# Kernel tuning notes

Measured on AMD Instinct MI355X. Metric: run time of the kernel, lower is better.

## Reference

```python
import jax, jax.numpy as jnp
import numpy as np

H, W = 512, 512
CHUNK = 128            # gaussians blended per scan step
BLUR = 0.3             # antialiasing dilation (as in 3DGS EWA low-pass)
ALPHA_MIN = 1.0 / 255.0
ALPHA_MAX = 0.99


def setup_inputs() -> dict:
    key = jax.random.key(0)
    k = jax.random.split(key, 6)
    N = 8192
    means2D = jax.random.uniform(k[0], (N, 2), jnp.float32) * jnp.array([W, H], jnp.float32)
    colors = jax.random.uniform(k[1], (N, 3), jnp.float32)
    opacities = jax.random.uniform(k[2], (N, 1), jnp.float32)
    scales = jax.random.uniform(k[3], (N, 2), jnp.float32) * 15.0 + 1.0   # pixels
    rotations = jax.random.uniform(k[4], (N, 1), jnp.float32) * (2.0 * np.pi)
    depths = jax.random.uniform(k[5], (N,), jnp.float32)
    background = jnp.zeros((3,), jnp.float32)
    return dict(means2D=means2D, colors=colors, opacities=opacities,
                scales=scales, rotations=rotations, depths=depths,
                background=background)


def _rasterize(means2D, colors, opacities, scales, rotations, depths, background):
    # depth sort: front (small depth) first
    order = jnp.argsort(depths)
    m = means2D[order]                 # [N,2] (x,y)
    col = colors[order]                # [N,3]
    op = opacities[order][:, 0]        # [N]
    s = scales[order]                  # [N,2]
    th = rotations[order][:, 0]        # [N]

    # 2D covariance  Sigma = R diag(s^2) R^T
    c, si = jnp.cos(th), jnp.sin(th)
    sx2, sy2 = s[:, 0] ** 2, s[:, 1] ** 2
    A = c * c * sx2 + si * si * sy2
    Cc = si * si * sx2 + c * c * sy2
    B = c * si * (sx2 - sy2)
    det = A * Cc - B * B
    # antialiasing: dilate covariance, compensate opacity
    A2, C2 = A + BLUR, Cc + BLUR
    det2 = A2 * C2 - B * B
    op = op * jnp.sqrt(jnp.maximum(det / det2, 0.0))
    invdet = 1.0 / det2
    ia, ib, ic = C2 * invdet, -B * invdet, A2 * invdet   # Sigma^-1 entries

    # pixel centers
    ys, xs = jnp.meshgrid(jnp.arange(H, dtype=jnp.float32) + 0.5,
                          jnp.arange(W, dtype=jnp.float32) + 0.5, indexing='ij')

    N = m.shape[0]
    nchunk = N // CHUNK
    chunk = lambda a: a.reshape((nchunk, CHUNK) + a.shape[1:])
    gs = (chunk(m), chunk(col), chunk(op), chunk(ia), chunk(ib), chunk(ic))

    def step(carry, g):
        T, acc = carry                       # T:[H,W] transmittance, acc:[3,H,W]
        gm, gcol, gop, gia, gib, gic = g     # per-chunk [C,...]
        dx = xs[None] - gm[:, 0, None, None]                 # [C,H,W]
        dy = ys[None] - gm[:, 1, None, None]
        power = (-0.5 * (gia[:, None, None] * dx * dx + gic[:, None, None] * dy * dy)
                 - gib[:, None, None] * dx * dy)
        alpha = jnp.minimum(ALPHA_MAX, gop[:, None, None] * jnp.exp(power))
        alpha = jnp.where(alpha < ALPHA_MIN, 0.0, alpha)     # skip tiny splats (as CUDA)
        one_m = 1.0 - alpha
        cum = jnp.cumprod(one_m, axis=0)                     # inclusive
        Twithin = jnp.concatenate([jnp.ones_like(cum[:1]), cum[:-1]], 0)  # exclusive
        w = alpha * Twithin * T[None]                        # blend weight per gaussian
        acc = acc + jnp.einsum('nc,nhw->chw', gcol, w)
        T = T * cum[-1]
        return (T, acc), None

    init = (jnp.ones((H, W), jnp.float32), jnp.zeros((3, H, W), jnp.float32))
    (T, acc), _ = jax.lax.scan(step, init, gs)
    color = acc + background[:, None, None] * T[None]        # [3,H,W]
    return color


def reference(means2D, colors, opacities, scales, rotations, depths, background):
    return _rasterize(means2D, colors, opacities, scales, rotations, depths, background)
```

## Files before the change

kernel.cpp:

```cpp
#include <hip/hip_runtime.h>
#include <hip/hip_fp16.h>
#include <stdint.h>

#define HH 512
#define WW 512
#define NPIX (HH*WW)
#define ALPHA_MIN_C (1.0f/255.0f)
#define ALPHA_MAX_C 0.99f
#define BLUR_C 0.3f
#define TERM_EPS 1.0e-4f
#define LOG2E 1.4426950408889634f

#define JSL 512
__global__ __launch_bounds__(256) void rank_kernel(const float* __restrict__ depths,
                                                   int N, int* __restrict__ partial) {
    __shared__ uint32_t sk[JSL];
    const int tid = threadIdx.x;
    const int ngb = N >> 8;
    const int gb = blockIdx.x % ngb;
    const int jb = blockIdx.x / ngb;
    const int j0 = jb * JSL;
    for (int i = tid; i < JSL; i += 256)
        sk[i] = __float_as_uint(depths[j0 + i]);
    __syncthreads();
    const int g = gb * 256 + tid;
    const uint32_t mb = __float_as_uint(depths[g]);
    const int glim = g - j0;
    int cnt = 0;
    const uint4* sk4 = (const uint4*)sk;
#pragma unroll 8
    for (int q = 0; q < JSL / 4; ++q) {
        uint4 v = sk4[q];
        const int i4 = q * 4;
        cnt += (v.x < mb) || (v.x == mb && (i4 + 0) < glim);
        cnt += (v.y < mb) || (v.y == mb && (i4 + 1) < glim);
        cnt += (v.z < mb) || (v.z == mb && (i4 + 2) < glim);
        cnt += (v.w < mb) || (v.w == mb && (i4 + 3) < glim);
    }
    partial[jb * N + g] = cnt;
}

__global__ __launch_bounds__(256) void prep_kernel(
    const float* __restrict__ means, const float* __restrict__ colors,
    const float* __restrict__ ops, const float* __restrict__ scales,
    const float* __restrict__ rots, const int* __restrict__ partial, int N,
    float4* __restrict__ pP, float4* __restrict__ pQ, float* __restrict__ pC) {
    int g = blockIdx.x * 256 + threadIdx.x;
    if (g >= N) return;
    int pos = 0;
#pragma unroll
    for (int s = 0; s < 16; ++s) pos += partial[s * N + g];
    float mx = means[2*g], my = means[2*g+1];
    float th = rots[g];
    float c = cosf(th), si = sinf(th);
    float sx = scales[2*g], sy = scales[2*g+1];
    float sx2 = sx*sx, sy2 = sy*sy;
    float A  = c*c*sx2 + si*si*sy2;
    float Cc = si*si*sx2 + c*c*sy2;
    float B  = c*si*(sx2 - sy2);
    float det = A*Cc - B*B;
    float A2 = A + BLUR_C, C2 = Cc + BLUR_C;
    float det2 = A2*C2 - B*B;
    float op = ops[g] * sqrtf(fmaxf(det/det2, 0.0f));
    float invd = 1.0f/det2;
    float ia = C2*invd, ib = -B*invd, ic = A2*invd;
    float iaF = -0.5f*LOG2E*ia, icF = -0.5f*LOG2E*ic, ibF = -LOG2E*ib;
    float bx, by, lop;
    if (op < ALPHA_MIN_C) {
        bx = -1.0f; by = -1.0f; lop = -128.0f;
    } else {
        float t = __logf(op * 255.0f);
        bx = sqrtf(fmaxf(2.0f * t * A2, 0.0f)) * 1.0001f + 0.1f;
        by = sqrtf(fmaxf(2.0f * t * C2, 0.0f)) * 1.0001f + 0.1f;
        lop = __log2f(op);
    }
    __half2 h2 = __floats2half2_rn(ibF, icF);
    unsigned ibic; __builtin_memcpy(&ibic, &h2, 4);
    __half2 cc = __floats2half2_rn(colors[3*g], colors[3*g+1]);
    unsigned crcg; __builtin_memcpy(&crcg, &cc, 4);
    pP[pos] = make_float4(mx, my, bx, by);
    pQ[pos] = make_float4(iaF, __uint_as_float(ibic), lop, __uint_as_float(crcg));
    pC[pos] = colors[3*g+2];
}

#define NSEG 8
#define SEGG 1024
#define CHK  128
#define NCHK (SEGG/CHK)

__device__ __forceinline__ uint2 packAT(float r, float g, float b, float t) {
    __half2 hrg = __floats2half2_rn(r, g);
    __half2 hbt = __floats2half2_rn(b, t);
    uint2 u;
    __builtin_memcpy(&u.x, &hrg, 4);
    __builtin_memcpy(&u.y, &hbt, 4);
    return u;
}

__global__ __launch_bounds__(128) void seg_blend_kernel(
    const float4* __restrict__ pP, const float4* __restrict__ pQ,
    const float* __restrict__ pC, uint2* __restrict__ segbuf) {
    __shared__ __align__(16) float sG[2][2][CHK*8];
    const int tid  = threadIdx.x;
    const int lane = tid & 63;
    const int wid  = tid >> 6;
    const int tile = blockIdx.x & 1023;
    const int seg  = ((int)blockIdx.x >> 10) * 2 + wid;
    const int tX = tile & 31, tY = tile >> 5;
    const int px = tX*16 + (lane & 15);
    const int py = tY*16 + (lane >> 4);
    const float fx = px + 0.5f, fy = py + 0.5f;
    const float x0 = tX*16 + 0.5f, x1 = x0 + 15.0f;
    const float y0 = tY*16 + 0.5f, y1 = y0 + 15.0f;
    const uint64_t lm = (1ull << lane) - 1ull;
    float T0=1.f,T1=1.f,T2=1.f,T3=1.f;
    float aR0=0.f,aG0=0.f,aB0=0.f;
    float aR1=0.f,aG1=0.f,aB1=0.f;
    float aR2=0.f,aG2=0.f,aB2=0.f;
    float aR3=0.f,aG3=0.f,aB3=0.f;
    const int gb = seg * SEGG;

    float4 a0 = pP[gb+lane],    q0 = pQ[gb+lane];    float c0f = pC[gb+lane];
    float4 a1 = pP[gb+64+lane], q1 = pQ[gb+64+lane]; float c1f = pC[gb+64+lane];
    int cntA = 0, cntB = 0;
    {
        float nx = fabsf(fminf(fmaxf(a0.x,x0),x1)-a0.x);
        float ny = fabsf(fminf(fmaxf(a0.y,y0),y1)-a0.y);
        bool f0 = (nx <= a0.z) & (ny <= a0.w);
        nx = fabsf(fminf(fmaxf(a1.x,x0),x1)-a1.x);
        ny = fabsf(fminf(fmaxf(a1.y,y0),y1)-a1.y);
        bool f1 = (nx <= a1.z) & (ny <= a1.w);
        uint64_t m0 = __ballot(f0);
        if (f0) { float* rec = &sG[wid][0][__popcll(m0 & lm)*8];
                  *(float4*)rec = make_float4(a0.x,a0.y,q0.x,q0.y);
                  *(float4*)(rec+4) = make_float4(q0.z,q0.w,c0f,0.f); }
        int c0 = (int)__popcll(m0);
        uint64_t m1 = __ballot(f1);
        if (f1) { float* rec = &sG[wid][0][(c0 + __popcll(m1 & lm))*8];
                  *(float4*)rec = make_float4(a1.x,a1.y,q1.x,q1.y);
                  *(float4*)(rec+4) = make_float4(q1.z,q1.w,c1f,0.f); }
        cntA = c0 + (int)__popcll(m1);
    }
    {   const int g = gb + CHK + lane;
        a0 = pP[g]; q0 = pQ[g]; c0f = pC[g];
        a1 = pP[g+64]; q1 = pQ[g+64]; c1f = pC[g+64]; }

    int cur = 0;
    for (int k = 0; k < NCHK; ++k) {
        const int nxt = cur ^ 1;
        if (k + 1 < NCHK) {
            float nx = fabsf(fminf(fmaxf(a0.x,x0),x1)-a0.x);
            float ny = fabsf(fminf(fmaxf(a0.y,y0),y1)-a0.y);
            bool f0 = (nx <= a0.z) & (ny <= a0.w);
            nx = fabsf(fminf(fmaxf(a1.x,x0),x1)-a1.x);
            ny = fabsf(fminf(fmaxf(a1.y,y0),y1)-a1.y);
            bool f1 = (nx <= a1.z) & (ny <= a1.w);
            uint64_t m0 = __ballot(f0);
            if (f0) { float* rec = &sG[wid][nxt][__popcll(m0 & lm)*8];
                      *(float4*)rec = make_float4(a0.x,a0.y,q0.x,q0.y);
                      *(float4*)(rec+4) = make_float4(q0.z,q0.w,c0f,0.f); }
            int c0 = (int)__popcll(m0);
            uint64_t m1 = __ballot(f1);
            if (f1) { float* rec = &sG[wid][nxt][(c0 + __popcll(m1 & lm))*8];
                      *(float4*)rec = make_float4(a1.x,a1.y,q1.x,q1.y);
                      *(float4*)(rec+4) = make_float4(q1.z,q1.w,c1f,0.f); }
            const int cn = c0 + (int)__popcll(m1);
            if (nxt == 0) cntA = cn; else cntB = cn;
            if (k + 2 < NCHK) {
                const int g = gb + (k+2)*CHK + lane;
                a0 = pP[g]; q0 = pQ[g]; c0f = pC[g];
                a1 = pP[g+64]; q1 = pQ[g+64]; c1f = pC[g+64];
            }
        }
        const int cnt = (cur == 0) ? cntA : cntB;
        const float* segp = sG[wid][cur];
#pragma unroll 2
        for (int i = 0; i < cnt; ++i) {
            const float4 r0 = *(const float4*)(segp + i*8);
            const float4 r1 = *(const float4*)(segp + i*8 + 4);
            float dx = fx - r0.x;
            float dy = fy - r0.y;
            unsigned hh = __float_as_uint(r0.w);
            __half2 h2; __builtin_memcpy(&h2, &hh, 4);
            float ibv = __half2float(h2.x);
            float icv = __half2float(h2.y);
            float bse = fmaf(r0.z, dx*dx, r1.x);
            float pb  = ibv * dx;
            float d1 = dy + 4.0f, d2 = dy + 8.0f, d3 = dy + 12.0f;
            float p0 = fmaf(icv, dy*dy, fmaf(pb, dy, bse));
            float p1 = fmaf(icv, d1*d1, fmaf(pb, d1, bse));
            float p2 = fmaf(icv, d2*d2, fmaf(pb, d2, bse));
            float p3 = fmaf(icv, d3*d3, fmaf(pb, d3, bse));
            float al0 = fminf(ALPHA_MAX_C, exp2f(p0));
            float al1 = fminf(ALPHA_MAX_C, exp2f(p1));
            float al2 = fminf(ALPHA_MAX_C, exp2f(p2));
            float al3 = fminf(ALPHA_MAX_C, exp2f(p3));
            al0 = (al0 >= ALPHA_MIN_C) ? al0 : 0.0f;
            al1 = (al1 >= ALPHA_MIN_C) ? al1 : 0.0f;
            al2 = (al2 >= ALPHA_MIN_C) ? al2 : 0.0f;
            al3 = (al3 >= ALPHA_MIN_C) ? al3 : 0.0f;
            if (__any((al0 > 0.f) | (al1 > 0.f) | (al2 > 0.f) | (al3 > 0.f))) {
                unsigned cu = __float_as_uint(r1.y);
                __half2 ch; __builtin_memcpy(&ch, &cu, 4);
                float cr = __half2float(ch.x);
                float cg = __half2float(ch.y);
                float cb = r1.z;
                float s0 = al0*T0, s1 = al1*T1, s2 = al2*T2, s3 = al3*T3;
                aR0 = fmaf(cr,s0,aR0); aG0 = fmaf(cg,s0,aG0); aB0 = fmaf(cb,s0,aB0);
                aR1 = fmaf(cr,s1,aR1); aG1 = fmaf(cg,s1,aG1); aB1 = fmaf(cb,s1,aB1);
                aR2 = fmaf(cr,s2,aR2); aG2 = fmaf(cg,s2,aG2); aB2 = fmaf(cb,s2,aB2);
                aR3 = fmaf(cr,s3,aR3); aG3 = fmaf(cg,s3,aG3); aB3 = fmaf(cb,s3,aB3);
                T0 = fmaf(-al0,T0,T0); T1 = fmaf(-al1,T1,T1);
                T2 = fmaf(-al2,T2,T2); T3 = fmaf(-al3,T3,T3);
            }
        }
        if (__all((T0 < TERM_EPS) & (T1 < TERM_EPS) &
                  (T2 < TERM_EPS) & (T3 < TERM_EPS))) break;
        cur = nxt;
    }
    const int pix0 = py*WW + px;
    uint2* sb = segbuf + seg * NPIX;
    sb[pix0        ] = packAT(aR0, aG0, aB0, T0);
    sb[pix0 +  4*WW] = packAT(aR1, aG1, aB1, T1);
    sb[pix0 +  8*WW] = packAT(aR2, aG2, aB2, T2);
    sb[pix0 + 12*WW] = packAT(aR3, aG3, aB3, T3);
}

__global__ __launch_bounds__(256) void composite_kernel(
    const uint2* __restrict__ segbuf, const float* __restrict__ bg,
    float* __restrict__ out) {
    const int pix = blockIdx.x * 256 + threadIdx.x;
    float R = 0.f, G = 0.f, B = 0.f, T = 1.f;
#pragma unroll
    for (int s = 0; s < NSEG; ++s) {
        uint2 v = segbuf[s * NPIX + pix];
        __half2 hrg, hbt;
        __builtin_memcpy(&hrg, &v.x, 4);
        __builtin_memcpy(&hbt, &v.y, 4);
        R = fmaf(T, __half2float(hrg.x), R);
        G = fmaf(T, __half2float(hrg.y), G);
        B = fmaf(T, __half2float(hbt.x), B);
        T *= __half2float(hbt.y);
    }
    out[pix]          = R + bg[0]*T;
    out[pix +   NPIX] = G + bg[1]*T;
    out[pix + 2*NPIX] = B + bg[2]*T;
}

extern "C" void kernel_launch(void* const* d_in, const int* in_sizes, int n_in,
                              void* d_out, int out_size, void* d_ws, size_t ws_size,
                              hipStream_t stream) {
    const float* means   = (const float*)d_in[0];
    const float* colors  = (const float*)d_in[1];
    const float* ops     = (const float*)d_in[2];
    const float* scales  = (const float*)d_in[3];
    const float* rots    = (const float*)d_in[4];
    const float* depths  = (const float*)d_in[5];
    const float* bg      = (const float*)d_in[6];
    const int N = in_sizes[0] / 2;

    char* ws = (char*)d_ws;
    float4* pP    = (float4*)(ws);
    float4* pQ    = (float4*)(ws + (size_t)N*16);
    float*  pC    = (float*) (ws + (size_t)N*32);
    int*    part  = (int*)  (ws + (size_t)N*36);
    uint2*  segb  = (uint2*)(ws + (size_t)N*36 + (size_t)16*N*4);

    const int ngb = N / 256;
    const int njb = N / JSL;
    rank_kernel<<<dim3(ngb*njb), dim3(256), 0, stream>>>(depths, N, part);
    prep_kernel<<<dim3((N+255)/256), dim3(256), 0, stream>>>(
        means, colors, ops, scales, rots, part, N, pP, pQ, pC);
    seg_blend_kernel<<<dim3(4*1024), dim3(128), 0, stream>>>(pP, pQ, pC, segb);
    composite_kernel<<<dim3(NPIX/256), dim3(256), 0, stream>>>(
        segb, bg, (float*)d_out);
}
```

Measured before the change: 132.5 us.

## Bin gaussians into per-tile bitmasks via atomics instead of per-tile culling scan

Adds a binning kernel that, for each gaussian, sets a bit in a per-(segment, tile) 1024-bit mask using atomicOr over the 16x16 tiles its bounding box covers. The blend kernel then compacts the mask into an index list in shared memory and only loads the listed gaussians, with a one-ahead prefetch from global memory. This removes the per-tile culling of every gaussian in the segment. The cost is a memset, an extra kernel with atomics, indirect global loads, one wave per block, and loss of the early-termination check.

```diff
diff --git a/kernel.cpp b/kernel.cpp
--- a/kernel.cpp
+++ b/kernel.cpp
@@ -8,7 +8,6 @@
 #define ALPHA_MIN_C (1.0f/255.0f)
 #define ALPHA_MAX_C 0.99f
 #define BLUR_C 0.3f
-#define TERM_EPS 1.0e-4f
 #define LOG2E 1.4426950408889634f
 
 #define JSL 512
@@ -44,7 +43,7 @@
     const float* __restrict__ means, const float* __restrict__ colors,
     const float* __restrict__ ops, const float* __restrict__ scales,
     const float* __restrict__ rots, const int* __restrict__ partial, int N,
-    float4* __restrict__ pP, float4* __restrict__ pQ, float* __restrict__ pC) {
+    float4* __restrict__ pP, float4* __restrict__ pR0, float4* __restrict__ pR1) {
     int g = blockIdx.x * 256 + threadIdx.x;
     if (g >= N) return;
     int pos = 0;
@@ -78,15 +77,33 @@
     unsigned ibic; __builtin_memcpy(&ibic, &h2, 4);
     __half2 cc = __floats2half2_rn(colors[3*g], colors[3*g+1]);
     unsigned crcg; __builtin_memcpy(&crcg, &cc, 4);
-    pP[pos] = make_float4(mx, my, bx, by);
-    pQ[pos] = make_float4(iaF, __uint_as_float(ibic), lop, __uint_as_float(crcg));
-    pC[pos] = colors[3*g+2];
+    pP [pos] = make_float4(mx, my, bx, by);
+    pR0[pos] = make_float4(mx, my, iaF, __uint_as_float(ibic));
+    pR1[pos] = make_float4(lop, __uint_as_float(crcg), colors[3*g+2], 0.0f);
 }
 
 #define NSEG 8
 #define SEGG 1024
-#define CHK  128
-#define NCHK (SEGG/CHK)
+
+__global__ __launch_bounds__(256) void bin_kernel(
+    const float4* __restrict__ pP, uint32_t* __restrict__ masks, int N) {
+    int p = blockIdx.x * 256 + threadIdx.x;
+    if (p >= N) return;
+    float4 a = pP[p];
+    if (a.z < 0.0f) return;
+    int tx0 = max(0,  (int)ceilf ((a.x - a.z - 15.5f) * 0.0625f));
+    int tx1 = min(31, (int)floorf((a.x + a.z -  0.5f) * 0.0625f));
+    int ty0 = max(0,  (int)ceilf ((a.y - a.w - 15.5f) * 0.0625f));
+    int ty1 = min(31, (int)floorf((a.y + a.w -  0.5f) * 0.0625f));
+    const int seg = p >> 10;
+    const int bit = p & 1023;
+    const uint32_t wi = bit >> 5;
+    const uint32_t bm = 1u << (bit & 31);
+    uint32_t* base = masks + (((uint32_t)seg << 10) * 32) + wi;
+    for (int ty = ty0; ty <= ty1; ++ty)
+        for (int tx = tx0; tx <= tx1; ++tx)
+            atomicOr(base + (uint32_t)(ty*32 + tx) * 32, bm);
+}
 
 __device__ __forceinline__ uint2 packAT(float r, float g, float b, float t) {
     __half2 hrg = __floats2half2_rn(r, g);
@@ -97,87 +114,52 @@
     return u;
 }
 
-__global__ __launch_bounds__(128) void seg_blend_kernel(
-    const float4* __restrict__ pP, const float4* __restrict__ pQ,
-    const float* __restrict__ pC, uint2* __restrict__ segbuf) {
-    __shared__ __align__(16) float sG[2][2][CHK*8];
-    const int tid  = threadIdx.x;
-    const int lane = tid & 63;
-    const int wid  = tid >> 6;
+__global__ __launch_bounds__(64) void seg_blend_kernel(
+    const float4* __restrict__ pR0, const float4* __restrict__ pR1,
+    const uint32_t* __restrict__ masks, uint2* __restrict__ segbuf) {
+    __shared__ uint16_t sIdx[SEGG];
+    const int lane = threadIdx.x;
     const int tile = blockIdx.x & 1023;
-    const int seg  = ((int)blockIdx.x >> 10) * 2 + wid;
+    const int seg  = blockIdx.x >> 10;
     const int tX = tile & 31, tY = tile >> 5;
     const int px = tX*16 + (lane & 15);
     const int py = tY*16 + (lane >> 4);
     const float fx = px + 0.5f, fy = py + 0.5f;
-    const float x0 = tX*16 + 0.5f, x1 = x0 + 15.0f;
-    const float y0 = tY*16 + 0.5f, y1 = y0 + 15.0f;
-    const uint64_t lm = (1ull << lane) - 1ull;
+
+    uint32_t w = (lane < 32) ? masks[(((uint32_t)seg << 10) | tile)*32 + lane] : 0u;
+    int pc = __popc(w);
+    int inc = pc;
+#pragma unroll
+    for (int d = 1; d < 64; d <<= 1) {
+        int t = __shfl_up(inc, d);
+        if (lane >= d) inc += t;
+    }
+    const int M = __shfl(inc, 63);
+    int off = inc - pc;
+    const int bword = lane << 5;
+    while (w) {
+        int b = __ffs(w) - 1;
+        w &= w - 1;
+        sIdx[off++] = (uint16_t)(bword + b);
+    }
+    __threadfence_block();
+
     float T0=1.f,T1=1.f,T2=1.f,T3=1.f;
     float aR0=0.f,aG0=0.f,aB0=0.f;
     float aR1=0.f,aG1=0.f,aB1=0.f;
     float aR2=0.f,aG2=0.f,aB2=0.f;
     float aR3=0.f,aG3=0.f,aB3=0.f;
-    const int gb = seg * SEGG;
-
-    float4 a0 = pP[gb+lane],    q0 = pQ[gb+lane];    float c0f = pC[gb+lane];
-    float4 a1 = pP[gb+64+lane], q1 = pQ[gb+64+lane]; float c1f = pC[gb+64+lane];
-    int cntA = 0, cntB = 0;
-    {
-        float nx = fabsf(fminf(fmaxf(a0.x,x0),x1)-a0.x);
-        float ny = fabsf(fminf(fmaxf(a0.y,y0),y1)-a0.y);
-        bool f0 = (nx <= a0.z) & (ny <= a0.w);
-        nx = fabsf(fminf(fmaxf(a1.x,x0),x1)-a1.x);
-        ny = fabsf(fminf(fmaxf(a1.y,y0),y1)-a1.y);
-        bool f1 = (nx <= a1.z) & (ny <= a1.w);
-        uint64_t m0 = __ballot(f0);
-        if (f0) { float* rec = &sG[wid][0][__popcll(m0 & lm)*8];
-                  *(float4*)rec = make_float4(a0.x,a0.y,q0.x,q0.y);
-                  *(float4*)(rec+4) = make_float4(q0.z,q0.w,c0f,0.f); }
-        int c0 = (int)__popcll(m0);
-        uint64_t m1 = __ballot(f1);
-        if (f1) { float* rec = &sG[wid][0][(c0 + __popcll(m1 & lm))*8];
-                  *(float4*)rec = make_float4(a1.x,a1.y,q1.x,q1.y);
-                  *(float4*)(rec+4) = make_float4(q1.z,q1.w,c1f,0.f); }
-        cntA = c0 + (int)__popcll(m1);
-    }
-    {   const int g = gb + CHK + lane;
-        a0 = pP[g]; q0 = pQ[g]; c0f = pC[g];
-        a1 = pP[g+64]; q1 = pQ[g+64]; c1f = pC[g+64]; }
-
-    int cur = 0;
-    for (int k = 0; k < NCHK; ++k) {
-        const int nxt = cur ^ 1;
-        if (k + 1 < NCHK) {
-            float nx = fabsf(fminf(fmaxf(a0.x,x0),x1)-a0.x);
-            float ny = fabsf(fminf(fmaxf(a0.y,y0),y1)-a0.y);
-            bool f0 = (nx <= a0.z) & (ny <= a0.w);
-            nx = fabsf(fminf(fmaxf(a1.x,x0),x1)-a1.x);
-            ny = fabsf(fminf(fmaxf(a1.y,y0),y1)-a1.y);
-            bool f1 = (nx <= a1.z) & (ny <= a1.w);
-            uint64_t m0 = __ballot(f0);
-            if (f0) { float* rec = &sG[wid][nxt][__popcll(m0 & lm)*8];
-                      *(float4*)rec = make_float4(a0.x,a0.y,q0.x,q0.y);
-                      *(float4*)(rec+4) = make_float4(q0.z,q0.w,c0f,0.f); }
-            int c0 = (int)__popcll(m0);
-            uint64_t m1 = __ballot(f1);
-            if (f1) { float* rec = &sG[wid][nxt][(c0 + __popcll(m1 & lm))*8];
-                      *(float4*)rec = make_float4(a1.x,a1.y,q1.x,q1.y);
-                      *(float4*)(rec+4) = make_float4(q1.z,q1.w,c1f,0.f); }
-            const int cn = c0 + (int)__popcll(m1);
-            if (nxt == 0) cntA = cn; else cntB = cn;
-            if (k + 2 < NCHK) {
-                const int g = gb + (k+2)*CHK + lane;
-                a0 = pP[g]; q0 = pQ[g]; c0f = pC[g];
-                a1 = pP[g+64]; q1 = pQ[g+64]; c1f = pC[g+64];
-            }
-        }
-        const int cnt = (cur == 0) ? cntA : cntB;
-        const float* segp = sG[wid][cur];
-#pragma unroll 2
-        for (int i = 0; i < cnt; ++i) {
-            const float4 r0 = *(const float4*)(segp + i*8);
-            const float4 r1 = *(const float4*)(segp + i*8 + 4);
+    const int gb = seg << 10;
+
+    if (M > 0) {
+        int gi = gb + sIdx[0];
+        float4 r0 = pR0[gi];
+        float4 r1 = pR1[gi];
+        for (int i = 0; i < M; ++i) {
+            int giN = gi;
+            if (i + 1 < M) giN = gb + sIdx[i + 1];
+            float4 r0N = pR0[giN];
+            float4 r1N = pR1[giN];
             float dx = fx - r0.x;
             float dy = fy - r0.y;
             unsigned hh = __float_as_uint(r0.w);
@@ -213,10 +195,8 @@
                 T0 = fmaf(-al0,T0,T0); T1 = fmaf(-al1,T1,T1);
                 T2 = fmaf(-al2,T2,T2); T3 = fmaf(-al3,T3,T3);
             }
+            r0 = r0N; r1 = r1N; gi = giN;
         }
-        if (__all((T0 < TERM_EPS) & (T1 < TERM_EPS) &
-                  (T2 < TERM_EPS) & (T3 < TERM_EPS))) break;
-        cur = nxt;
     }
     const int pix0 = py*WW + px;
     uint2* sb = segbuf + seg * NPIX;
@@ -260,18 +240,22 @@
     const int N = in_sizes[0] / 2;
 
     char* ws = (char*)d_ws;
-    float4* pP    = (float4*)(ws);
-    float4* pQ    = (float4*)(ws + (size_t)N*16);
-    float*  pC    = (float*) (ws + (size_t)N*32);
-    int*    part  = (int*)  (ws + (size_t)N*36);
-    uint2*  segb  = (uint2*)(ws + (size_t)N*36 + (size_t)16*N*4);
+    float4*   pP    = (float4*)(ws);
+    float4*   pR0   = (float4*)(ws + (size_t)N*16);
+    float4*   pR1   = (float4*)(ws + (size_t)N*32);
+    int*      part  = (int*)   (ws + (size_t)N*48);
+    uint32_t* masks = (uint32_t*)(ws + (size_t)N*112);
+    uint2*    segb  = (uint2*) (ws + (size_t)N*112 + (size_t)NSEG*1024*128);
+
+    hipMemsetAsync(masks, 0, (size_t)NSEG*1024*128, stream);
 
     const int ngb = N / 256;
     const int njb = N / JSL;
     rank_kernel<<<dim3(ngb*njb), dim3(256), 0, stream>>>(depths, N, part);
     prep_kernel<<<dim3((N+255)/256), dim3(256), 0, stream>>>(
-        means, colors, ops, scales, rots, part, N, pP, pQ, pC);
-    seg_blend_kernel<<<dim3(4*1024), dim3(128), 0, stream>>>(pP, pQ, pC, segb);
+        means, colors, ops, scales, rots, part, N, pP, pR0, pR1);
+    bin_kernel<<<dim3((N+255)/256), dim3(256), 0, stream>>>(pP, masks, N);
+    seg_blend_kernel<<<dim3(NSEG*1024), dim3(64), 0, stream>>>(pR0, pR1, masks, segb);
     composite_kernel<<<dim3(NPIX/256), dim3(256), 0, stream>>>(
         segb, bg, (float*)d_out);
 }
```

After: 137.4 us. 3.7% more time.
